# Kernel tuning notes

Hardware: AMD Instinct MI355X
Metric: run time of the kernel (lower is better)

## Reference

```python
import jax, jax.numpy as jnp
import numpy as np

DIM = 768
HEADS = 12
DIM_HEAD = 64
INNER = HEADS * DIM_HEAD  # 768
B, N = 8, 1024


def layernorm(x, gamma, beta, eps=1e-5):
    mu = jnp.mean(x, axis=-1, keepdims=True)
    var = jnp.var(x, axis=-1, keepdims=True)
    return (x - mu) * jax.lax.rsqrt(var + eps) * gamma + beta


def setup_inputs() -> dict:
    key = jax.random.key(0)
    ks = jax.random.split(key, 12)
    s = lambda fan_in: 1.0 / np.sqrt(fan_in)
    return {
        "x": jax.random.normal(ks[0], (B, N, DIM), dtype=jnp.float32),
        "ln1_g": jnp.ones((DIM,), jnp.float32),
        "ln1_b": jnp.zeros((DIM,), jnp.float32),
        "ln2_g": jnp.ones((DIM,), jnp.float32),
        "ln2_b": jnp.zeros((DIM,), jnp.float32),
        "w_qkv": jax.random.uniform(ks[1], (DIM, 3 * INNER), jnp.float32, -s(DIM), s(DIM)),
        "w_out": jax.random.uniform(ks[2], (INNER, DIM), jnp.float32, -s(INNER), s(INNER)),
        "b_out": jax.random.uniform(ks[3], (DIM,), jnp.float32, -s(INNER), s(INNER)),
        "w_ff1": jax.random.uniform(ks[4], (DIM, 4 * DIM), jnp.float32, -s(DIM), s(DIM)),
        "b_ff1": jax.random.uniform(ks[5], (4 * DIM,), jnp.float32, -s(DIM), s(DIM)),
        "w_ff2": jax.random.uniform(ks[6], (4 * DIM, DIM), jnp.float32, -s(4 * DIM), s(4 * DIM)),
        "b_ff2": jax.random.uniform(ks[7], (DIM,), jnp.float32, -s(4 * DIM), s(4 * DIM)),
    }


def reference(x, ln1_g, ln1_b, ln2_g, ln2_b, w_qkv, w_out, b_out, w_ff1, b_ff1, w_ff2, b_ff2):
    # --- attention sub-block (dropout = identity, eval mode) ---
    residual = x
    h = layernorm(x, ln1_g, ln1_b)
    qkv = h @ w_qkv  # [B, N, 3*INNER]
    q, k, v = jnp.split(qkv, 3, axis=-1)
    # b n (h d) -> b h n d
    reshape = lambda t: t.reshape(B, N, HEADS, DIM_HEAD).transpose(0, 2, 1, 3)
    q, k, v = reshape(q), reshape(k), reshape(v)
    scale = DIM_HEAD ** -0.5
    attn = jnp.einsum('bhnd,bhmd->bhnm', q, k) * scale
    attn = jax.nn.softmax(attn, axis=-1)
    out = jnp.einsum('bhnm,bhmd->bhnd', attn, v)
    out = out.transpose(0, 2, 1, 3).reshape(B, N, INNER)  # b h n d -> b n (h d)
    out = out @ w_out + b_out
    x = residual + out
    # --- FFN sub-block ---
    h2 = layernorm(x, ln2_g, ln2_b)
    ff = jax.nn.gelu(h2 @ w_ff1 + b_ff1, approximate=False) @ w_ff2 + b_ff2
    return x + ff
```

## Files before the change

kernel.cpp:

```cpp
#include <hip/hip_runtime.h>
#include <hip/hip_bf16.h>
#include <math.h>
#include <stdint.h>

#define BATCH 8
#define SEQ   1024
#define DIM   768
#define HEADS 12
#define DHEAD 64
#define TOK   (BATCH*SEQ)
#define INNER 768
#define FFDIM 3072
#define QKVN  2304
#define QKLD  1536

typedef float floatx4 __attribute__((ext_vector_type(4)));
typedef __bf16 bf16x8 __attribute__((ext_vector_type(8)));

__device__ __forceinline__ float b2f(uint16_t u) {
    return __uint_as_float(((uint32_t)u) << 16);
}
__device__ __forceinline__ uint16_t f2b(float f) {
    uint32_t x = __float_as_uint(f);
    x += 0x7fffu + ((x >> 16) & 1u);
    return (uint16_t)(x >> 16);
}
__device__ __forceinline__ uint32_t cvt_pk_bf16(float lo, float hi) {
    uint32_t r;
    asm("v_cvt_pk_bf16_f32 %0, %1, %2" : "=v"(r) : "v"(lo), "v"(hi));
    return r;
}
__device__ __forceinline__ float exp2_fast(float x) {
    float r; asm("v_exp_f32 %0, %1" : "=v"(r) : "v"(x)); return r;
}
__device__ __forceinline__ float rcp_fast(float x) {
    float r; asm("v_rcp_f32 %0, %1" : "=v"(r) : "v"(x)); return r;
}

__device__ __forceinline__ float gelu_exact(float v) {
    float x  = v * 0.70710678f;
    float ax = fabsf(x);
    float t  = rcp_fast(fmaf(0.3275911f, ax, 1.0f));
    float poly = t * fmaf(t, fmaf(t, fmaf(t, fmaf(t, 1.061405429f, -1.453152027f),
                          1.421413741f), -0.284496736f), 0.254829592f);
    float e = 1.0f - poly * exp2_fast(x * x * -1.44269504f);
    float erfv = copysignf(e, x);
    return 0.5f * v * (1.0f + erfv);
}

__device__ __forceinline__ void gload_lds16(const uint16_t* g, uint16_t* l) {
    __builtin_amdgcn_global_load_lds(
        (const __attribute__((address_space(1))) uint32_t*)g,
        (__attribute__((address_space(3))) uint32_t*)l, 16, 0, 0);
}

__global__ __launch_bounds__(256) void transpose_all(
    const float* __restrict__ w_qkv, const float* __restrict__ w_out,
    const float* __restrict__ w_ff1, const float* __restrict__ w_ff2,
    uint16_t* __restrict__ WqT, uint16_t* __restrict__ WoT,
    uint16_t* __restrict__ W1T, uint16_t* __restrict__ W2T)
{
    __shared__ float tile[32][33];
    int bid = blockIdx.x;
    const float* in; uint16_t* outp; int R, C, tx, ty;
    if (bid < 1728)      { in = w_qkv; outp = WqT; R = 768;  C = 2304; tx = bid % 72;            ty = bid / 72; }
    else if (bid < 2304) { int q = bid - 1728; in = w_out; outp = WoT; R = 768;  C = 768;  tx = q % 24; ty = q / 24; }
    else if (bid < 4608) { int q = bid - 2304; in = w_ff1; outp = W1T; R = 768;  C = 3072; tx = q % 96; ty = q / 96; }
    else                 { int q = bid - 4608; in = w_ff2; outp = W2T; R = 3072; C = 768;  tx = q % 24; ty = q / 24; }
    int c0 = tx * 32, r0 = ty * 32;
    int x = threadIdx.x;
    int y = threadIdx.y;
    #pragma unroll
    for (int i = y; i < 32; i += 8)
        tile[i][x] = in[(size_t)(r0 + i) * C + c0 + x];
    __syncthreads();
    #pragma unroll
    for (int i = y; i < 32; i += 8)
        outp[(size_t)(c0 + i) * R + r0 + x] = f2b(tile[x][i]);
}

__global__ __launch_bounds__(256) void ln_naive(
    const float* __restrict__ x, const float* __restrict__ g,
    const float* __restrict__ be, uint16_t* __restrict__ y)
{
    const int lane = threadIdx.x & 63;
    const size_t row = blockIdx.x * 4 + (threadIdx.x >> 6);
    float v[12];
    float s = 0.f, ss = 0.f;
    #pragma unroll
    for (int j = 0; j < 12; j++) {
        int idx = lane + j * 64;
        float f = x[row * DIM + idx];
        v[j] = f; s += f; ss += f * f;
    }
    #pragma unroll
    for (int off = 32; off > 0; off >>= 1) {
        s  += __shfl_xor(s, off);
        ss += __shfl_xor(ss, off);
    }
    const float mu = s * (1.f / DIM);
    const float var = ss * (1.f / DIM) - mu * mu;
    const float rstd = rsqrtf(var + 1e-5f);
    #pragma unroll
    for (int j = 0; j < 12; j++) {
        int idx = lane + j * 64;
        y[row * DIM + idx] = f2b((v[j] - mu) * rstd * g[idx] + be[idx]);
    }
}

#define GEMM_STAGE(buf, kk) do {                                                            \
    _Pragma("unroll")                                                                       \
    for (int i = 0; i < 2; i++) {                                                           \
        int row = i * 64 + srow;                                                            \
        gload_lds16(A  + (size_t)(tileM + row) * lda  + (kk) + scol, &a_s[buf][row * 32 + scol]); \
        gload_lds16(Bt + (size_t)(tileN + row) * ldbt + (kk) + scol, &b_s[buf][row * 32 + scol]); \
    } } while (0)

template<bool BIAS, bool GELU, bool RES, bool OUTF, bool VSPLIT>
__global__ __launch_bounds__(256) void gemm_bt(
    const uint16_t* __restrict__ A, const uint16_t* __restrict__ Bt,
    void* C, const float* __restrict__ bias, int bias_off,
    const float* res, int N, int K, int lda, int ldbt, int ldc,
    uint16_t* __restrict__ vt)
{
    __shared__ __align__(16) uint16_t a_s[3][128 * 32];
    __shared__ __align__(16) uint16_t b_s[3][128 * 32];
    const int tid = threadIdx.x;
    const int wave = tid >> 6, lane = tid & 63;
    const int wr = wave >> 1, wc = wave & 1;

    const int nwg = gridDim.x * gridDim.y;
    int bid = blockIdx.y * gridDim.x + blockIdx.x;
    if ((nwg & 7) == 0)
        bid = (bid & 7) * (nwg >> 3) + (bid >> 3);
    const int tileM = (bid / gridDim.x) * 128;
    const int tileN = (bid % gridDim.x) * 128;

    floatx4 acc[4][4] = {};

    const int scol = (tid & 3) * 8;
    const int srow = tid >> 2;
    const int lm = lane & 15;
    const int lq = lane >> 4;
    const int kq = lq * 8;

    const int nt = K >> 5;

    GEMM_STAGE(0, 0);
    GEMM_STAGE(1, 32);

    int rd = 0, st = 2;
    for (int t = 0; t < nt; ++t) {
        if (t == nt - 1) asm volatile("s_waitcnt vmcnt(0)" ::: "memory");
        else             asm volatile("s_waitcnt vmcnt(4)" ::: "memory");
        __builtin_amdgcn_s_barrier();
        __builtin_amdgcn_sched_barrier(0);

        if (t + 2 < nt) GEMM_STAGE(st, (t + 2) * 32);

        bf16x8 af[4], bfr[4];
        #pragma unroll
        for (int rt = 0; rt < 4; rt++) {
            int r = wr * 64 + rt * 16 + lm;
            af[rt] = *(const bf16x8*)&a_s[rd][r * 32 + kq];
        }
        #pragma unroll
        for (int ntt = 0; ntt < 4; ntt++) {
            int n = wc * 64 + ntt * 16 + lm;
            bfr[ntt] = *(const bf16x8*)&b_s[rd][n * 32 + kq];
        }
        #pragma unroll
        for (int rt = 0; rt < 4; rt++)
            #pragma unroll
            for (int ntt = 0; ntt < 4; ntt++)
                acc[rt][ntt] = __builtin_amdgcn_mfma_f32_16x16x32_bf16(
                    af[rt], bfr[ntt], acc[rt][ntt], 0, 0, 0);

        rd = rd + 1; if (rd == 3) rd = 0;
        st = st + 1; if (st == 3) st = 0;
    }

    const bool vpath = VSPLIT && (tileN >= 1536);
    #pragma unroll
    for (int rt = 0; rt < 4; rt++) {
        int r0 = tileM + wr * 64 + rt * 16 + lq * 4;
        #pragma unroll
        for (int ntt = 0; ntt < 4; ntt++) {
            int cg = tileN + wc * 64 + ntt * 16 + lm;
            if (vpath) {
                int d = cg - 1536;
                int bb = r0 >> 10, s0 = r0 & 1023;
                uint32_t p0 = (uint32_t)f2b(acc[rt][ntt][0]) | ((uint32_t)f2b(acc[rt][ntt][1]) << 16);
                uint32_t p1 = (uint32_t)f2b(acc[rt][ntt][2]) | ((uint32_t)f2b(acc[rt][ntt][3]) << 16);
                uint2 pk; pk.x = p0; pk.y = p1;
                *(uint2*)&vt[((size_t)bb * 768 + d) * 1024 + s0] = pk;
            } else {
                float bvv = BIAS ? bias[bias_off + cg] : 0.f;
                #pragma unroll
                for (int r = 0; r < 4; r++) {
                    float v = acc[rt][ntt][r] + bvv;
                    if (GELU) v = gelu_exact(v);
                    size_t ci = (size_t)(r0 + r) * ldc + cg;
                    if (RES) v += res[ci];
                    if (OUTF) ((float*)C)[ci] = v;
                    else      ((uint16_t*)C)[ci] = f2b(v);
                }
            }
        }
    }
}

#define KSWZ(row, cb) ((cb) ^ (((row) & 7) << 4))
#define NKT (SEQ / 64)
#define SM_C   0.18033688f
#define SM_THR 11.5416f

__global__ __launch_bounds__(512) void flash_mfma(
    uint16_t* qk, const uint16_t* __restrict__ vt)
{
    __shared__ __align__(16) uint16_t k_s[2][64 * 64];
    __shared__ __align__(16) uint16_t v_s[2][64 * 64];
    __shared__ __align__(16) uint16_t p_s[128 * 64];
    char* k_base = (char*)k_s;
    char* v_base = (char*)v_s;
    char* p_c    = (char*)p_s;

    const int t = threadIdx.x;
    const int wq = t >> 6;
    const int lane = t & 63;
    const int lm = lane & 15;
    const int lq = lane >> 4;

    int flat = blockIdx.x + 8 * (blockIdx.y + 12 * blockIdx.z);
    int nw = (flat & 7) * 96 + (flat >> 3);
    const int b   = nw / 96;
    const int rem = nw - b * 96;
    const int h   = rem >> 3;
    const int qb  = rem & 7;

    const size_t rowbase = (size_t)b * SEQ;
    const int hcol = h * DHEAD;

    bf16x8 qf[2];
    {
        const uint16_t* qp = qk + (rowbase + qb*128 + wq*16 + lm) * QKLD + hcol + lq*8;
        qf[0] = *(const bf16x8*)qp;
        qf[1] = *(const bf16x8*)(qp + 32);
    }

    floatx4 O[4] = {};
    float m_q = -1e30f, l_q = 0.f;

    const int s_row = t >> 3;
    const int s_cb  = (t & 7) * 16;
    const size_t kgbase = (rowbase + s_row) * QKLD + INNER + hcol;
    const size_t vgbase = ((size_t)b * 768 + hcol + s_row) * 1024;

    uint4 kr0, vr0;
    {
        kr0 = *(const uint4*)((const char*)(qk + kgbase) + s_cb);
        vr0 = *(const uint4*)((const char*)(vt + vgbase) + s_cb);
        *(uint4*)&k_base[s_row*128 + KSWZ(s_row, s_cb)] = kr0;
        *(uint4*)&v_base[s_row*128 + KSWZ(s_row, s_cb)] = vr0;
    }

    int cur = 0;
    for (int kt = 0; kt < NKT; ++kt) {
        __syncthreads();

        if (kt + 1 < NKT) {
            kr0 = *(const uint4*)((const char*)(qk + kgbase + (size_t)(kt + 1) * 64 * QKLD) + s_cb);
            vr0 = *(const uint4*)((const char*)(vt + vgbase + (size_t)(kt + 1) * 64) + s_cb);
        }

        const char* k_c = k_base + cur * 8192;
        const char* v_c = v_base + cur * 8192;

        floatx4 S[4];
        __builtin_amdgcn_s_setprio(1);
        #pragma unroll
        for (int nt = 0; nt < 4; nt++) {
            const int row = nt*16 + lm;
            bf16x8 ak0 = *(const bf16x8*)&k_c[row*128 + KSWZ(row, lq*16)];
            bf16x8 ak1 = *(const bf16x8*)&k_c[row*128 + KSWZ(row, 64 + lq*16)];
            floatx4 a = {};
            a = __builtin_amdgcn_mfma_f32_16x16x32_bf16(ak0, qf[0], a, 0, 0, 0);
            a = __builtin_amdgcn_mfma_f32_16x16x32_bf16(ak1, qf[1], a, 0, 0, 0);
            S[nt] = a;
        }
        __builtin_amdgcn_s_setprio(0);

        float m0 = fmaxf(fmaxf(S[0][0], S[0][1]), fmaxf(S[0][2], S[0][3]));
        float m1 = fmaxf(fmaxf(S[1][0], S[1][1]), fmaxf(S[1][2], S[1][3]));
        float m2 = fmaxf(fmaxf(S[2][0], S[2][1]), fmaxf(S[2][2], S[2][3]));
        float m3 = fmaxf(fmaxf(S[3][0], S[3][1]), fmaxf(S[3][2], S[3][3]));
        float mx = fmaxf(fmaxf(m0, m1), fmaxf(m2, m3)) * SM_C;
        mx = fmaxf(mx, __shfl_xor(mx, 16));
        mx = fmaxf(mx, __shfl_xor(mx, 32));

        float mn = m_q;
        if (!__all(mx <= m_q + SM_THR)) {
            mn = fmaxf(m_q, mx);
            float alpha = exp2_fast(m_q - mn);
            m_q = mn;
            l_q *= alpha;
            #pragma unroll
            for (int nt = 0; nt < 4; nt++) {
                O[nt][0] *= alpha; O[nt][1] *= alpha;
                O[nt][2] *= alpha; O[nt][3] *= alpha;
            }
        }

        float p[4][4];
        float sum = 0.f;
        #pragma unroll
        for (int nt = 0; nt < 4; nt++) {
            float p0 = exp2_fast(fmaf(S[nt][0], SM_C, -mn));
            float p1 = exp2_fast(fmaf(S[nt][1], SM_C, -mn));
            float p2 = exp2_fast(fmaf(S[nt][2], SM_C, -mn));
            float p3 = exp2_fast(fmaf(S[nt][3], SM_C, -mn));
            p[nt][0] = p0; p[nt][1] = p1; p[nt][2] = p2; p[nt][3] = p3;
            sum += (p0 + p1) + (p2 + p3);
        }
        sum += __shfl_xor(sum, 16);
        sum += __shfl_xor(sum, 32);
        l_q += sum;

        const int prow = wq*16 + lm;
        #pragma unroll
        for (int nt = 0; nt < 4; nt++) {
            uint2 w;
            w.x = cvt_pk_bf16(p[nt][0], p[nt][1]);
            w.y = cvt_pk_bf16(p[nt][2], p[nt][3]);
            *(uint2*)&p_c[prow*128 + KSWZ(prow, nt*32 + lq*8)] = w;
        }

        __builtin_amdgcn_s_setprio(1);
        #pragma unroll
        for (int ks = 0; ks < 2; ks++) {
            bf16x8 bp = *(const bf16x8*)&p_c[prow*128 + KSWZ(prow, ks*64 + lq*16)];
            #pragma unroll
            for (int nt = 0; nt < 4; nt++) {
                const int vrow = nt*16 + lm;
                bf16x8 av = *(const bf16x8*)&v_c[vrow*128 + KSWZ(vrow, ks*64 + lq*16)];
                O[nt] = __builtin_amdgcn_mfma_f32_16x16x32_bf16(av, bp, O[nt], 0, 0, 0);
            }
        }
        __builtin_amdgcn_s_setprio(0);

        if (kt + 1 < NKT) {
            char* kn = k_base + (cur ^ 1) * 8192;
            char* vn = v_base + (cur ^ 1) * 8192;
            *(uint4*)&kn[s_row*128 + KSWZ(s_row, s_cb)] = kr0;
            *(uint4*)&vn[s_row*128 + KSWZ(s_row, s_cb)] = vr0;
        }
        cur ^= 1;
    }

    const float linv = rcp_fast(l_q);
    uint16_t* dst = qk + (rowbase + qb*128 + wq*16 + lm) * QKLD + hcol;
    #pragma unroll
    for (int nt = 0; nt < 4; nt++) {
        uint2 w;
        w.x = cvt_pk_bf16(O[nt][0] * linv, O[nt][1] * linv);
        w.y = cvt_pk_bf16(O[nt][2] * linv, O[nt][3] * linv);
        *(uint2*)&dst[nt*16 + lq*4] = w;
    }
}

extern "C" void kernel_launch(void* const* d_in, const int* in_sizes, int n_in,
                              void* d_out, int out_size, void* d_ws, size_t ws_size,
                              hipStream_t stream) {
    const float* x      = (const float*)d_in[0];
    const float* ln1_g  = (const float*)d_in[1];
    const float* ln1_b  = (const float*)d_in[2];
    const float* ln2_g  = (const float*)d_in[3];
    const float* ln2_b  = (const float*)d_in[4];
    const float* w_qkv  = (const float*)d_in[5];
    const float* w_out  = (const float*)d_in[6];
    const float* b_out  = (const float*)d_in[7];
    const float* w_ff1  = (const float*)d_in[8];
    const float* b_ff1  = (const float*)d_in[9];
    const float* w_ff2  = (const float*)d_in[10];
    const float* b_ff2  = (const float*)d_in[11];
    float* out = (float*)d_out;

    uint16_t* ws  = (uint16_t*)d_ws;
    uint16_t* qk  = ws;
    uint16_t* ffc = ws;
    uint16_t* vT  = ws + (size_t)12582912;
    uint16_t* h   = ws + (size_t)18874368;
    uint16_t* WqT = ws + (size_t)25165824;
    uint16_t* WoT = ws + (size_t)26935296;
    uint16_t* W1T = ws + (size_t)27525120;
    uint16_t* W2T = ws + (size_t)29884416;

    hipLaunchKernelGGL(transpose_all, dim3(6912), dim3(32, 8), 0, stream,
                       w_qkv, w_out, w_ff1, w_ff2, WqT, WoT, W1T, W2T);

    hipLaunchKernelGGL(ln_naive, dim3(TOK/4), dim3(256), 0, stream, x, ln1_g, ln1_b, h);
    hipLaunchKernelGGL((gemm_bt<false, false, false, false, true>), dim3(QKVN/128, TOK/128), dim3(256), 0, stream,
                       h, WqT, qk, nullptr, 0, nullptr, QKVN, DIM, DIM, DIM, QKLD, vT);
    hipLaunchKernelGGL(flash_mfma, dim3(SEQ/128, HEADS, BATCH), dim3(512), 0, stream, qk, vT);
    hipLaunchKernelGGL((gemm_bt<true, false, true, true, false>), dim3(DIM/128, TOK/128), dim3(256), 0, stream,
                       qk, WoT, out, b_out, 0, x, DIM, INNER, QKLD, DIM, DIM, nullptr);
    hipLaunchKernelGGL(ln_naive, dim3(TOK/4), dim3(256), 0, stream, out, ln2_g, ln2_b, h);
    for (int c = 0; c < 2; c++) {
        hipLaunchKernelGGL((gemm_bt<true, true, false, false, false>), dim3(1536/128, TOK/128), dim3(256), 0, stream,
                           h, W1T + (size_t)c*1536*DIM, ffc, b_ff1, c*1536, nullptr,
                           1536, DIM, DIM, DIM, 1536, nullptr);
        if (c == 0) {
            hipLaunchKernelGGL((gemm_bt<true, false, true, true, false>), dim3(DIM/128, TOK/128), dim3(256), 0, stream,
                               ffc, W2T + (size_t)c*1536, out, b_ff2, 0, out,
                               DIM, 1536, 1536, FFDIM, DIM, nullptr);
        } else {
            hipLaunchKernelGGL((gemm_bt<false, false, true, true, false>), dim3(DIM/128, TOK/128), dim3(256), 0, stream,
                               ffc, W2T + (size_t)c*1536, out, nullptr, 0, out,
                               DIM, 1536, 1536, FFDIM, DIM, nullptr);
        }
    }
}
```

Measured before the change: 412.0 us.

## Replace direct global-to-LDS triple buffering with register-staged double buffering

The GEMM main loop stops using global_load_lds with a three-stage LDS ring and manual vmcnt waits. It now prefetches the next K-tile into registers, computes on the current LDS buffer, and writes the prefetched data into the other LDS buffer, with one __syncthreads per iteration. This halves prefetch depth and LDS use and frees the compiler to schedule loads, but it adds register pressure and LDS write traffic, and the loads now have only one tile of compute to hide behind.

```diff
diff --git a/kernel.cpp b/kernel.cpp
--- a/kernel.cpp
+++ b/kernel.cpp
@@ -46,12 +46,6 @@
     float e = 1.0f - poly * exp2_fast(x * x * -1.44269504f);
     float erfv = copysignf(e, x);
     return 0.5f * v * (1.0f + erfv);
-}
-
-__device__ __forceinline__ void gload_lds16(const uint16_t* g, uint16_t* l) {
-    __builtin_amdgcn_global_load_lds(
-        (const __attribute__((address_space(1))) uint32_t*)g,
-        (__attribute__((address_space(3))) uint32_t*)l, 16, 0, 0);
 }
 
 __global__ __launch_bounds__(256) void transpose_all(
@@ -108,14 +102,6 @@
     }
 }
 
-#define GEMM_STAGE(buf, kk) do {                                                            \
-    _Pragma("unroll")                                                                       \
-    for (int i = 0; i < 2; i++) {                                                           \
-        int row = i * 64 + srow;                                                            \
-        gload_lds16(A  + (size_t)(tileM + row) * lda  + (kk) + scol, &a_s[buf][row * 32 + scol]); \
-        gload_lds16(Bt + (size_t)(tileN + row) * ldbt + (kk) + scol, &b_s[buf][row * 32 + scol]); \
-    } } while (0)
-
 template<bool BIAS, bool GELU, bool RES, bool OUTF, bool VSPLIT>
 __global__ __launch_bounds__(256) void gemm_bt(
     const uint16_t* __restrict__ A, const uint16_t* __restrict__ Bt,
@@ -123,8 +109,8 @@
     const float* res, int N, int K, int lda, int ldbt, int ldc,
     uint16_t* __restrict__ vt)
 {
-    __shared__ __align__(16) uint16_t a_s[3][128 * 32];
-    __shared__ __align__(16) uint16_t b_s[3][128 * 32];
+    __shared__ __align__(16) uint16_t a_s[2][128 * 32];
+    __shared__ __align__(16) uint16_t b_s[2][128 * 32];
     const int tid = threadIdx.x;
     const int wave = tid >> 6, lane = tid & 63;
     const int wr = wave >> 1, wc = wave & 1;
@@ -144,30 +130,45 @@
     const int lq = lane >> 4;
     const int kq = lq * 8;
 
+    const uint16_t* Ab0 = A  + (size_t)(tileM + srow) * lda;
+    const uint16_t* Ab1 = A  + (size_t)(tileM + 64 + srow) * lda;
+    const uint16_t* Bb0 = Bt + (size_t)(tileN + srow) * ldbt;
+    const uint16_t* Bb1 = Bt + (size_t)(tileN + 64 + srow) * ldbt;
+
     const int nt = K >> 5;
 
-    GEMM_STAGE(0, 0);
-    GEMM_STAGE(1, 32);
-
-    int rd = 0, st = 2;
+    uint4 ar0, ar1, br0, br1;
+    ar0 = *(const uint4*)(Ab0 + scol);
+    ar1 = *(const uint4*)(Ab1 + scol);
+    br0 = *(const uint4*)(Bb0 + scol);
+    br1 = *(const uint4*)(Bb1 + scol);
+    *(uint4*)&a_s[0][srow * 32 + scol]        = ar0;
+    *(uint4*)&a_s[0][(64 + srow) * 32 + scol] = ar1;
+    *(uint4*)&b_s[0][srow * 32 + scol]        = br0;
+    *(uint4*)&b_s[0][(64 + srow) * 32 + scol] = br1;
+
+    int cur = 0;
     for (int t = 0; t < nt; ++t) {
-        if (t == nt - 1) asm volatile("s_waitcnt vmcnt(0)" ::: "memory");
-        else             asm volatile("s_waitcnt vmcnt(4)" ::: "memory");
-        __builtin_amdgcn_s_barrier();
-        __builtin_amdgcn_sched_barrier(0);
-
-        if (t + 2 < nt) GEMM_STAGE(st, (t + 2) * 32);
+        __syncthreads();
+
+        if (t + 1 < nt) {
+            const int kk = (t + 1) * 32 + scol;
+            ar0 = *(const uint4*)(Ab0 + kk);
+            ar1 = *(const uint4*)(Ab1 + kk);
+            br0 = *(const uint4*)(Bb0 + kk);
+            br1 = *(const uint4*)(Bb1 + kk);
+        }
 
         bf16x8 af[4], bfr[4];
         #pragma unroll
         for (int rt = 0; rt < 4; rt++) {
             int r = wr * 64 + rt * 16 + lm;
-            af[rt] = *(const bf16x8*)&a_s[rd][r * 32 + kq];
+            af[rt] = *(const bf16x8*)&a_s[cur][r * 32 + kq];
         }
         #pragma unroll
         for (int ntt = 0; ntt < 4; ntt++) {
             int n = wc * 64 + ntt * 16 + lm;
-            bfr[ntt] = *(const bf16x8*)&b_s[rd][n * 32 + kq];
+            bfr[ntt] = *(const bf16x8*)&b_s[cur][n * 32 + kq];
         }
         #pragma unroll
         for (int rt = 0; rt < 4; rt++)
@@ -176,8 +177,13 @@
                 acc[rt][ntt] = __builtin_amdgcn_mfma_f32_16x16x32_bf16(
                     af[rt], bfr[ntt], acc[rt][ntt], 0, 0, 0);
 
-        rd = rd + 1; if (rd == 3) rd = 0;
-        st = st + 1; if (st == 3) st = 0;
+        if (t + 1 < nt) {
+            *(uint4*)&a_s[cur ^ 1][srow * 32 + scol]        = ar0;
+            *(uint4*)&a_s[cur ^ 1][(64 + srow) * 32 + scol] = ar1;
+            *(uint4*)&b_s[cur ^ 1][srow * 32 + scol]        = br0;
+            *(uint4*)&b_s[cur ^ 1][(64 + srow) * 32 + scol] = br1;
+        }
+        cur ^= 1;
     }
 
     const bool vpath = VSPLIT && (tileN >= 1536);
```

Measured after the change: 403.1 us. -2.2%, faster.
